# Kernel tuning notes

Hardware: AMD Instinct MI355X
Metric: run time of the kernel (lower is better)

## Reference

```python
import jax, jax.numpy as jnp
import numpy as np

NEG = -1e6  # masked_softmax fill value from the torch source


def setup_inputs() -> dict:
    key = jax.random.key(0)
    ks = jax.random.split(key, 7)
    B, NQ, NK, D, H = 4, 256, 1024, 256, 256
    queries = jax.random.normal(ks[0], (B, NQ, D), dtype=jnp.float32)
    keys_ = jax.random.normal(ks[1], (B, NK, D), dtype=jnp.float32)
    values = jax.random.normal(ks[2], (B, NK, D), dtype=jnp.float32)
    valid_lens = jax.random.randint(ks[3], (B,), 1, NK + 1, dtype=jnp.int32)
    scale = 1.0 / np.sqrt(D)
    Wq = jax.random.normal(ks[4], (D, H), dtype=jnp.float32) * scale
    Wk = jax.random.normal(ks[5], (D, H), dtype=jnp.float32) * scale
    w_v = jax.random.normal(ks[6], (H,), dtype=jnp.float32) * (1.0 / np.sqrt(H))
    return {"queries": queries, "keys": keys_, "values": values,
            "valid_lens": valid_lens, "Wq": Wq, "Wk": Wk, "w_v": w_v}


def reference(queries, keys, values, valid_lens, Wq, Wk, w_v):
    # projections
    q = jnp.einsum('bqd,dh->bqh', queries, Wq)           # [B,NQ,H]
    k = jnp.einsum('bkd,dh->bkh', keys, Wk)              # [B,NK,H]
    # broadcast-add + tanh + dense(->1): scores [B,NQ,NK]
    features = jnp.tanh(q[:, :, None, :] + k[:, None, :, :])  # [B,NQ,NK,H]
    scores = jnp.einsum('bqkh,h->bqk', features, w_v)
    # masked softmax over last axis with per-batch valid lengths
    nk = keys.shape[1]
    mask = jnp.arange(nk)[None, None, :] < valid_lens[:, None, None]  # [B,1,NK]
    scores = jnp.where(mask, scores, NEG)
    attn = jax.nn.softmax(scores, axis=-1)               # [B,NQ,NK]
    # dropout in eval mode -> identity
    return jnp.einsum('bqk,bkd->bqd', attn, values)      # [B,NQ,D]
```

## Files before the change

kernel.cpp:

```cpp
#include <hip/hip_runtime.h>
#include <math.h>

#define BB 4
#define NQ 256
#define NK 1024
#define DD 256
#define HH 256

#define TM 64
#define TN 64
#define TKK 16
#define NT (DD / TKK)

__global__ __launch_bounds__(256) void proj_tanh_kernel(
    const float* __restrict__ Q, const float* __restrict__ K,
    const float* __restrict__ Wq, const float* __restrict__ Wk,
    float* __restrict__ tq, float* __restrict__ tk)
{
    const int QTILES = (BB * NQ) / TM;
    int bx = blockIdx.x;
    const float* A; const float* W; float* C; int bm;
    if (bx < QTILES) { A = Q; W = Wq; C = tq; bm = bx * TM; }
    else             { A = K; W = Wk; C = tk; bm = (bx - QTILES) * TM; }
    int bn = blockIdx.y * TN;

    __shared__ float As[2][TKK][TM + 4];
    __shared__ float Ws[2][TKK][TN + 4];

    int tid = threadIdx.x;
    int ar = tid >> 2, ac4 = tid & 3;
    int wkk = tid >> 4, wc4 = tid & 15;
    int ty = tid >> 4, tx = tid & 15;

    float4 aR = *(const float4*)&A[(size_t)(bm + ar) * DD + ac4 * 4];
    float4 wR = *(const float4*)&W[(size_t)wkk * HH + bn + wc4 * 4];

    float acc[4][4] = {};

    for (int t = 0; t < NT; ++t) {
        int cur = t & 1;
        As[cur][ac4 * 4 + 0][ar] = aR.x;
        As[cur][ac4 * 4 + 1][ar] = aR.y;
        As[cur][ac4 * 4 + 2][ar] = aR.z;
        As[cur][ac4 * 4 + 3][ar] = aR.w;
        *(float4*)&Ws[cur][wkk][wc4 * 4] = wR;
        if (t + 1 < NT) {
            int k0 = (t + 1) * TKK;
            aR = *(const float4*)&A[(size_t)(bm + ar) * DD + k0 + ac4 * 4];
            wR = *(const float4*)&W[(size_t)(k0 + wkk) * HH + bn + wc4 * 4];
        }
        __syncthreads();
#pragma unroll
        for (int kk = 0; kk < TKK; ++kk) {
            float4 a4 = *(const float4*)&As[cur][kk][ty * 4];
            float4 w4 = *(const float4*)&Ws[cur][kk][tx * 4];
            acc[0][0] = fmaf(a4.x, w4.x, acc[0][0]);
            acc[0][1] = fmaf(a4.x, w4.y, acc[0][1]);
            acc[0][2] = fmaf(a4.x, w4.z, acc[0][2]);
            acc[0][3] = fmaf(a4.x, w4.w, acc[0][3]);
            acc[1][0] = fmaf(a4.y, w4.x, acc[1][0]);
            acc[1][1] = fmaf(a4.y, w4.y, acc[1][1]);
            acc[1][2] = fmaf(a4.y, w4.z, acc[1][2]);
            acc[1][3] = fmaf(a4.y, w4.w, acc[1][3]);
            acc[2][0] = fmaf(a4.z, w4.x, acc[2][0]);
            acc[2][1] = fmaf(a4.z, w4.y, acc[2][1]);
            acc[2][2] = fmaf(a4.z, w4.z, acc[2][2]);
            acc[2][3] = fmaf(a4.z, w4.w, acc[2][3]);
            acc[3][0] = fmaf(a4.w, w4.x, acc[3][0]);
            acc[3][1] = fmaf(a4.w, w4.y, acc[3][1]);
            acc[3][2] = fmaf(a4.w, w4.z, acc[3][2]);
            acc[3][3] = fmaf(a4.w, w4.w, acc[3][3]);
        }
    }

#pragma unroll
    for (int i = 0; i < 4; ++i) {
        int m = bm + ty * 4 + i;
        float4 o;
        float t0 = tanhf(acc[i][0]), t1 = tanhf(acc[i][1]);
        float t2 = tanhf(acc[i][2]), t3 = tanhf(acc[i][3]);
        o.x = fminf(fmaxf(t0, -0.999999f), 0.999999f);
        o.y = fminf(fmaxf(t1, -0.999999f), 0.999999f);
        o.z = fminf(fmaxf(t2, -0.999999f), 0.999999f);
        o.w = fminf(fmaxf(t3, -0.999999f), 0.999999f);
        *(float4*)&C[(size_t)m * HH + bn + tx * 4] = o;
    }
}

__device__ __forceinline__ float pairterm(float a1, float b1, float w1,
                                          float a2, float b2, float w2, float acc) {
    float d1 = fmaf(a1, b1, 1.f);
    float d2 = fmaf(a2, b2, 1.f);
    float n1 = w1 * (a1 + b1);
    float n2 = w2 * (a2 + b2);
    float num = fmaf(n2, d1, n1 * d2);
    return fmaf(num, __builtin_amdgcn_rcpf(d1 * d2), acc);
}
__device__ __forceinline__ float pair2(float4 A, float4 B, float4 w, float acc) {
    acc = pairterm(A.x, B.x, w.x, A.y, B.y, w.y, acc);
    acc = pairterm(A.z, B.z, w.z, A.w, B.w, w.w, acc);
    return acc;
}

__global__ __launch_bounds__(256) void scores_kernel(
    const float* __restrict__ tq, const float* __restrict__ tk,
    const float* __restrict__ wv, const int* __restrict__ vlen,
    float* __restrict__ St, float* __restrict__ Psum)
{
    __shared__ __align__(16) float sQ[32][HH + 4];
    __shared__ __align__(16) float sK[32][HH + 4];
    __shared__ __align__(16) float sW[HH];

    int bid = blockIdx.x;
    int b = bid & 3;
    int rest = bid >> 2;
    int qc = rest & 7;
    int kc = rest >> 3;
    int L = vlen[b];
    int k0 = kc * 32;
    if (k0 >= L) return;
    int q0 = qc * 32;

    int tid = threadIdx.x;
    {
        int c4 = tid & 63, r0 = tid >> 6;
        const float4* gq = (const float4*)(tq + ((size_t)b * NQ + q0) * HH);
        const float4* gk = (const float4*)(tk + ((size_t)b * NK + k0) * HH);
#pragma unroll
        for (int r = 0; r < 32; r += 4) {
            *(float4*)&sQ[r + r0][c4 * 4] = gq[(size_t)(r + r0) * (HH / 4) + c4];
            *(float4*)&sK[r + r0][c4 * 4] = gk[(size_t)(r + r0) * (HH / 4) + c4];
        }
        sW[tid] = wv[tid];
    }
    __syncthreads();

    int ki = tid & 15, qi = tid >> 4;
    float a00 = 0.f, a01 = 0.f, a10 = 0.f, a11 = 0.f;
    const float4* qp0 = (const float4*)&sQ[qi][0];
    const float4* qp1 = (const float4*)&sQ[qi + 16][0];
    const float4* kp0 = (const float4*)&sK[ki][0];
    const float4* kp1 = (const float4*)&sK[ki + 16][0];
    const float4* wp  = (const float4*)sW;

#pragma unroll 4
    for (int h = 0; h < HH / 4; ++h) {
        float4 w4 = wp[h];
        float4 A0 = qp0[h], A1 = qp1[h];
        float4 B0 = kp0[h], B1 = kp1[h];
        a00 = pair2(A0, B0, w4, a00);
        a01 = pair2(A0, B1, w4, a01);
        a10 = pair2(A1, B0, w4, a10);
        a11 = pair2(A1, B1, w4, a11);
    }

    int kA = k0 + ki, kB = kA + 16;
    float p00 = (kA < L) ? __expf(a00) : 0.f;
    float p10 = (kA < L) ? __expf(a10) : 0.f;
    float p01 = (kB < L) ? __expf(a01) : 0.f;
    float p11 = (kB < L) ? __expf(a11) : 0.f;

    float* s0 = St + ((size_t)b * NQ + q0 + qi) * NK;
    float* s1 = St + ((size_t)b * NQ + q0 + qi + 16) * NK;
    s0[kA] = p00; s0[kB] = p01;
    s1[kA] = p10; s1[kB] = p11;

    float r0s = p00 + p01, r1s = p10 + p11;
#pragma unroll
    for (int o = 1; o <= 8; o <<= 1) {
        r0s += __shfl_xor(r0s, o, 64);
        r1s += __shfl_xor(r1s, o, 64);
    }
    if (ki == 0) {
        Psum[((size_t)b * NQ + q0 + qi) * 32 + kc] = r0s;
        Psum[((size_t)b * NQ + q0 + qi + 16) * 32 + kc] = r1s;
    }
}

__global__ __launch_bounds__(256) void pv_kernel(
    const float* __restrict__ St, const float* __restrict__ V,
    const float* __restrict__ Psum, const int* __restrict__ vlen,
    float* __restrict__ out)
{
    __shared__ __align__(16) float sPt[2][32][36];
    __shared__ __align__(16) float sV[2][32][36];
    __shared__ float sAll[3][64][17];
    __shared__ float sRowsum[32];

    int bid = blockIdx.x;
    int b = bid & 3;
    int rest = bid >> 2;
    int qt = rest >> 3, dt = rest & 7;
    int q0 = qt * 32, d0 = dt * 32;
    int L = vlen[b];
    int nc = (L + 31) >> 5;

    int tid = threadIdx.x;
    if (tid < 32) {
        float s = 0.f;
        const float* pp = Psum + ((size_t)b * NQ + q0 + tid) * 32;
        for (int c = 0; c < nc; ++c) s += pp[c];
        sRowsum[tid] = s;
    }

    int r = tid >> 3, c4 = tid & 7;
    int w = tid >> 6, sp = tid & 63;
    int qg = sp >> 3, dg = sp & 7;

    const float* Stb = St + ((size_t)b * NQ + q0 + r) * NK;
    const float* Vb  = V + (size_t)b * NK * DD + d0;

    float4 pf = *(const float4*)(Stb + c4 * 4);
    float4 vf = *(const float4*)(Vb + (size_t)r * DD + c4 * 4);

    float acc[4][4] = {};

    for (int c = 0; c < nc; ++c) {
        int cur = c & 1;
        sPt[cur][c4 * 4 + 0][r] = pf.x;
        sPt[cur][c4 * 4 + 1][r] = pf.y;
        sPt[cur][c4 * 4 + 2][r] = pf.z;
        sPt[cur][c4 * 4 + 3][r] = pf.w;
        *(float4*)&sV[cur][r][c4 * 4] = vf;
        if (c + 1 < nc) {
            int kn = (c + 1) * 32;
            pf = *(const float4*)(Stb + kn + c4 * 4);
            vf = *(const float4*)(Vb + (size_t)(kn + r) * DD + c4 * 4);
        }
        __syncthreads();
#pragma unroll
        for (int kk = 0; kk < 8; ++kk) {
            float4 A  = *(const float4*)&sPt[cur][w * 8 + kk][qg * 4];
            float4 Bv = *(const float4*)&sV[cur][w * 8 + kk][dg * 4];
            acc[0][0] = fmaf(A.x, Bv.x, acc[0][0]);
            acc[0][1] = fmaf(A.x, Bv.y, acc[0][1]);
            acc[0][2] = fmaf(A.x, Bv.z, acc[0][2]);
            acc[0][3] = fmaf(A.x, Bv.w, acc[0][3]);
            acc[1][0] = fmaf(A.y, Bv.x, acc[1][0]);
            acc[1][1] = fmaf(A.y, Bv.y, acc[1][1]);
            acc[1][2] = fmaf(A.y, Bv.z, acc[1][2]);
            acc[1][3] = fmaf(A.y, Bv.w, acc[1][3]);
            acc[2][0] = fmaf(A.z, Bv.x, acc[2][0]);
            acc[2][1] = fmaf(A.z, Bv.y, acc[2][1]);
            acc[2][2] = fmaf(A.z, Bv.z, acc[2][2]);
            acc[2][3] = fmaf(A.z, Bv.w, acc[2][3]);
            acc[3][0] = fmaf(A.w, Bv.x, acc[3][0]);
            acc[3][1] = fmaf(A.w, Bv.y, acc[3][1]);
            acc[3][2] = fmaf(A.w, Bv.z, acc[3][2]);
            acc[3][3] = fmaf(A.w, Bv.w, acc[3][3]);
        }
    }

    if (w > 0) {
#pragma unroll
        for (int i = 0; i < 4; ++i)
#pragma unroll
            for (int j = 0; j < 4; ++j) sAll[w - 1][sp][i * 4 + j] = acc[i][j];
    }
    __syncthreads();
    if (w == 0) {
#pragma unroll
        for (int ww = 0; ww < 3; ++ww)
#pragma unroll
            for (int i = 0; i < 4; ++i)
#pragma unroll
                for (int j = 0; j < 4; ++j) acc[i][j] += sAll[ww][sp][i * 4 + j];
#pragma unroll
        for (int i = 0; i < 4; ++i) {
            float inv = 1.0f / sRowsum[qg * 4 + i];
            float4 o = { acc[i][0] * inv, acc[i][1] * inv,
                         acc[i][2] * inv, acc[i][3] * inv };
            *(float4*)&out[((size_t)b * NQ + q0 + qg * 4 + i) * DD + d0 + dg * 4] = o;
        }
    }
}

extern "C" void kernel_launch(void* const* d_in, const int* in_sizes, int n_in,
                              void* d_out, int out_size, void* d_ws, size_t ws_size,
                              hipStream_t stream) {
    const float* queries = (const float*)d_in[0];
    const float* keys    = (const float*)d_in[1];
    const float* values  = (const float*)d_in[2];
    const int*   vlens   = (const int*)d_in[3];
    const float* Wq      = (const float*)d_in[4];
    const float* Wk      = (const float*)d_in[5];
    const float* wv      = (const float*)d_in[6];
    float* out = (float*)d_out;

    float* tq   = (float*)d_ws;
    float* tk   = tq + (size_t)BB * NQ * HH;
    float* St   = tk + (size_t)BB * NK * HH;
    float* Psum = St + (size_t)BB * NQ * NK;

    dim3 pgrid((BB * NQ) / TM + (BB * NK) / TM, HH / TN);
    proj_tanh_kernel<<<pgrid, 256, 0, stream>>>(queries, keys, Wq, Wk, tq, tk);

    scores_kernel<<<dim3(BB * (NQ / 32) * (NK / 32)), 256, 0, stream>>>(
        tq, tk, wv, vlens, St, Psum);

    pv_kernel<<<dim3(BB * (NQ / 32) * (DD / 32)), 256, 0, stream>>>(
        St, values, Psum, vlens, out);
}
```

Measured before the change: 60.64 us.

## Use exp-domain tanh identity, split H across blocks, add combine kernel

The projection epilogue now stores exp(2x), clamped, in place of tanh(x). The score kernel evaluates sum w*tanh(q+k) through the identity tanh(a+b) = 1 - 2/(1+e^{2a}e^{2b}), computed as rational pairs with one reciprocal per four h terms. The H dimension is split into four chunks over more 64x64 blocks, so partial sums go to a new buffer. A new combine kernel reduces those partials and applies exp and the row sums, and key tiles past the valid length are skipped in the projection. The cost is extra global traffic for the four partial score planes, one more launch, and clamping the pre-activation to ±8, which changes accuracy slightly.

```diff
diff --git a/kernel.cpp b/kernel.cpp
--- a/kernel.cpp
+++ b/kernel.cpp
@@ -12,16 +12,23 @@
 #define TKK 16
 #define NT (DD / TKK)
 
-__global__ __launch_bounds__(256) void proj_tanh_kernel(
+__global__ __launch_bounds__(256) void proj_exp_kernel(
     const float* __restrict__ Q, const float* __restrict__ K,
     const float* __restrict__ Wq, const float* __restrict__ Wk,
-    float* __restrict__ tq, float* __restrict__ tk)
+    const int* __restrict__ vlen,
+    float* __restrict__ Eq, float* __restrict__ Ek)
 {
     const int QTILES = (BB * NQ) / TM;
     int bx = blockIdx.x;
     const float* A; const float* W; float* C; int bm;
-    if (bx < QTILES) { A = Q; W = Wq; C = tq; bm = bx * TM; }
-    else             { A = K; W = Wk; C = tk; bm = (bx - QTILES) * TM; }
+    if (bx < QTILES) { A = Q; W = Wq; C = Eq; bm = bx * TM; }
+    else {
+        int kt = bx - QTILES;
+        int b = kt >> 4;
+        int lr = (kt & 15) * TM;
+        if (lr >= vlen[b]) return;
+        A = K; W = Wk; C = Ek; bm = kt * TM;
+    }
     int bn = blockIdx.y * TN;
 
     __shared__ float As[2][TKK][TM + 4];
@@ -71,121 +78,142 @@
             acc[3][2] = fmaf(a4.w, w4.z, acc[3][2]);
             acc[3][3] = fmaf(a4.w, w4.w, acc[3][3]);
         }
+        __syncthreads();
     }
 
 #pragma unroll
     for (int i = 0; i < 4; ++i) {
         int m = bm + ty * 4 + i;
         float4 o;
-        float t0 = tanhf(acc[i][0]), t1 = tanhf(acc[i][1]);
-        float t2 = tanhf(acc[i][2]), t3 = tanhf(acc[i][3]);
-        o.x = fminf(fmaxf(t0, -0.999999f), 0.999999f);
-        o.y = fminf(fmaxf(t1, -0.999999f), 0.999999f);
-        o.z = fminf(fmaxf(t2, -0.999999f), 0.999999f);
-        o.w = fminf(fmaxf(t3, -0.999999f), 0.999999f);
+        o.x = __expf(2.f * fminf(fmaxf(acc[i][0], -8.f), 8.f));
+        o.y = __expf(2.f * fminf(fmaxf(acc[i][1], -8.f), 8.f));
+        o.z = __expf(2.f * fminf(fmaxf(acc[i][2], -8.f), 8.f));
+        o.w = __expf(2.f * fminf(fmaxf(acc[i][3], -8.f), 8.f));
         *(float4*)&C[(size_t)m * HH + bn + tx * 4] = o;
     }
 }
 
-__device__ __forceinline__ float pairterm(float a1, float b1, float w1,
-                                          float a2, float b2, float w2, float acc) {
-    float d1 = fmaf(a1, b1, 1.f);
-    float d2 = fmaf(a2, b2, 1.f);
-    float n1 = w1 * (a1 + b1);
-    float n2 = w2 * (a2 + b2);
-    float num = fmaf(n2, d1, n1 * d2);
-    return fmaf(num, __builtin_amdgcn_rcpf(d1 * d2), acc);
-}
-__device__ __forceinline__ float pair2(float4 A, float4 B, float4 w, float acc) {
-    acc = pairterm(A.x, B.x, w.x, A.y, B.y, w.y, acc);
-    acc = pairterm(A.z, B.z, w.z, A.w, B.w, w.w, acc);
-    return acc;
-}
+#define SH 64
+#define NHC (HH / SH)
 
 __global__ __launch_bounds__(256) void scores_kernel(
-    const float* __restrict__ tq, const float* __restrict__ tk,
+    const float* __restrict__ Eq, const float* __restrict__ Ek,
     const float* __restrict__ wv, const int* __restrict__ vlen,
-    float* __restrict__ St, float* __restrict__ Psum)
+    float* __restrict__ Tpart)
 {
-    __shared__ __align__(16) float sQ[32][HH + 4];
-    __shared__ __align__(16) float sK[32][HH + 4];
-    __shared__ __align__(16) float sW[HH];
+    __shared__ __align__(16) float sQ[64][SH + 4];
+    __shared__ __align__(16) float sK[64][SH + 4];
+    __shared__ float sW[SH];
 
     int bid = blockIdx.x;
-    int b = bid & 3;
-    int rest = bid >> 2;
-    int qc = rest & 7;
-    int kc = rest >> 3;
+    int b  = bid & 3;
+    int qc = (bid >> 2) & 3;
+    int kc = (bid >> 4) & 15;
+    int hc = bid >> 8;
     int L = vlen[b];
-    int k0 = kc * 32;
+    int k0 = kc * 64;
     if (k0 >= L) return;
-    int q0 = qc * 32;
+    int q0 = qc * 64, h0 = hc * SH;
 
     int tid = threadIdx.x;
     {
-        int c4 = tid & 63, r0 = tid >> 6;
-        const float4* gq = (const float4*)(tq + ((size_t)b * NQ + q0) * HH);
-        const float4* gk = (const float4*)(tk + ((size_t)b * NK + k0) * HH);
-#pragma unroll
-        for (int r = 0; r < 32; r += 4) {
-            *(float4*)&sQ[r + r0][c4 * 4] = gq[(size_t)(r + r0) * (HH / 4) + c4];
-            *(float4*)&sK[r + r0][c4 * 4] = gk[(size_t)(r + r0) * (HH / 4) + c4];
-        }
-        sW[tid] = wv[tid];
+        int rr0 = tid >> 4;
+        int c4  = tid & 15;
+        const float* gq = Eq + ((size_t)b * NQ + q0) * HH + h0;
+        const float* gk = Ek + ((size_t)b * NK + k0) * HH + h0;
+#pragma unroll
+        for (int rr = 0; rr < 4; ++rr) {
+            int r = rr0 + rr * 16;
+            *(float4*)&sQ[r][c4 * 4] = *(const float4*)&gq[(size_t)r * HH + c4 * 4];
+            *(float4*)&sK[r][c4 * 4] = *(const float4*)&gk[(size_t)r * HH + c4 * 4];
+        }
+        if (tid < SH) sW[tid] = wv[h0 + tid];
     }
     __syncthreads();
 
-    int ki = tid & 15, qi = tid >> 4;
-    float a00 = 0.f, a01 = 0.f, a10 = 0.f, a11 = 0.f;
-    const float4* qp0 = (const float4*)&sQ[qi][0];
-    const float4* qp1 = (const float4*)&sQ[qi + 16][0];
-    const float4* kp0 = (const float4*)&sK[ki][0];
-    const float4* kp1 = (const float4*)&sK[ki + 16][0];
-    const float4* wp  = (const float4*)sW;
-
-#pragma unroll 4
-    for (int h = 0; h < HH / 4; ++h) {
-        float4 w4 = wp[h];
-        float4 A0 = qp0[h], A1 = qp1[h];
-        float4 B0 = kp0[h], B1 = kp1[h];
-        a00 = pair2(A0, B0, w4, a00);
-        a01 = pair2(A0, B1, w4, a01);
-        a10 = pair2(A1, B0, w4, a10);
-        a11 = pair2(A1, B1, w4, a11);
-    }
-
-    int kA = k0 + ki, kB = kA + 16;
-    float p00 = (kA < L) ? __expf(a00) : 0.f;
-    float p10 = (kA < L) ? __expf(a10) : 0.f;
-    float p01 = (kB < L) ? __expf(a01) : 0.f;
-    float p11 = (kB < L) ? __expf(a11) : 0.f;
-
-    float* s0 = St + ((size_t)b * NQ + q0 + qi) * NK;
-    float* s1 = St + ((size_t)b * NQ + q0 + qi + 16) * NK;
-    s0[kA] = p00; s0[kB] = p01;
-    s1[kA] = p10; s1[kB] = p11;
-
-    float r0s = p00 + p01, r1s = p10 + p11;
-#pragma unroll
-    for (int o = 1; o <= 8; o <<= 1) {
-        r0s += __shfl_xor(r0s, o, 64);
-        r1s += __shfl_xor(r1s, o, 64);
-    }
-    if (ki == 0) {
-        Psum[((size_t)b * NQ + q0 + qi) * 32 + kc] = r0s;
-        Psum[((size_t)b * NQ + q0 + qi + 16) * 32 + kc] = r1s;
-    }
+    int qi = tid >> 4, ki = tid & 15;
+    float acc[4][4] = {};
+
+    for (int h4 = 0; h4 < SH / 4; ++h4) {
+        float4 w = *(const float4*)&sW[h4 * 4];
+        float wxy = w.x + w.y, wzw = w.z + w.w;
+        float4 Aq[4], Bk[4];
+#pragma unroll
+        for (int i = 0; i < 4; ++i) Aq[i] = *(const float4*)&sQ[qi + 16 * i][h4 * 4];
+#pragma unroll
+        for (int j = 0; j < 4; ++j) Bk[j] = *(const float4*)&sK[ki + 16 * j][h4 * 4];
+#pragma unroll
+        for (int i = 0; i < 4; ++i)
+#pragma unroll
+            for (int j = 0; j < 4; ++j) {
+                float4 a = Aq[i], e = Bk[j];
+                float E1 = a.x * e.x, E2 = a.y * e.y;
+                float E3 = a.z * e.z, E4 = a.w * e.w;
+                float d1 = E1 + 1.f, d2 = E2 + 1.f;
+                float d3 = E3 + 1.f, d4 = E4 + 1.f;
+                float n12 = fmaf(w.x, E2, fmaf(w.y, E1, wxy));
+                float n34 = fmaf(w.z, E4, fmaf(w.w, E3, wzw));
+                float d12 = d1 * d2, d34 = d3 * d4;
+                float num = fmaf(n12, d34, n34 * d12);
+                acc[i][j] = fmaf(num, __builtin_amdgcn_rcpf(d12 * d34), acc[i][j]);
+            }
+    }
+
+    float* Tb = Tpart + (size_t)hc * (BB * NQ * NK)
+              + ((size_t)b * NQ + q0) * NK + k0;
+#pragma unroll
+    for (int i = 0; i < 4; ++i)
+#pragma unroll
+        for (int j = 0; j < 4; ++j)
+            Tb[(size_t)(qi + 16 * i) * NK + ki + 16 * j] = acc[i][j];
+}
+
+__global__ __launch_bounds__(256) void combine_kernel(
+    const float* __restrict__ Tpart, const int* __restrict__ vlen,
+    float* __restrict__ P, float* __restrict__ Psum)
+{
+    __shared__ float sRed[4];
+    int row = blockIdx.x;
+    int b = row >> 8;
+    int L = vlen[b];
+    int tid = threadIdx.x;
+    const size_t stride = (size_t)BB * NQ * NK;
+    const float* T0 = Tpart + (size_t)row * NK;
+
+    int k = tid * 4;
+    float4 p = {0.f, 0.f, 0.f, 0.f};
+    if (k < L) {
+        float4 t0 = *(const float4*)&T0[k];
+        float4 t1 = *(const float4*)&T0[stride + k];
+        float4 t2 = *(const float4*)&T0[2 * stride + k];
+        float4 t3 = *(const float4*)&T0[3 * stride + k];
+        float Tx = (t0.x + t1.x) + (t2.x + t3.x);
+        float Ty = (t0.y + t1.y) + (t2.y + t3.y);
+        float Tz = (t0.z + t1.z) + (t2.z + t3.z);
+        float Tw = (t0.w + t1.w) + (t2.w + t3.w);
+        p.x = __expf(-2.f * Tx);
+        p.y = (k + 1 < L) ? __expf(-2.f * Ty) : 0.f;
+        p.z = (k + 2 < L) ? __expf(-2.f * Tz) : 0.f;
+        p.w = (k + 3 < L) ? __expf(-2.f * Tw) : 0.f;
+    }
+    *(float4*)&P[(size_t)row * NK + k] = p;
+
+    float s = (p.x + p.y) + (p.z + p.w);
+#pragma unroll
+    for (int o = 32; o; o >>= 1) s += __shfl_xor(s, o, 64);
+    if ((tid & 63) == 0) sRed[tid >> 6] = s;
+    __syncthreads();
+    if (tid == 0) Psum[row] = (sRed[0] + sRed[1]) + (sRed[2] + sRed[3]);
 }
 
 __global__ __launch_bounds__(256) void pv_kernel(
-    const float* __restrict__ St, const float* __restrict__ V,
+    const float* __restrict__ P, const float* __restrict__ V,
     const float* __restrict__ Psum, const int* __restrict__ vlen,
     float* __restrict__ out)
 {
     __shared__ __align__(16) float sPt[2][32][36];
     __shared__ __align__(16) float sV[2][32][36];
     __shared__ float sAll[3][64][17];
-    __shared__ float sRowsum[32];
 
     int bid = blockIdx.x;
     int b = bid & 3;
@@ -196,21 +224,14 @@
     int nc = (L + 31) >> 5;
 
     int tid = threadIdx.x;
-    if (tid < 32) {
-        float s = 0.f;
-        const float* pp = Psum + ((size_t)b * NQ + q0 + tid) * 32;
-        for (int c = 0; c < nc; ++c) s += pp[c];
-        sRowsum[tid] = s;
-    }
-
     int r = tid >> 3, c4 = tid & 7;
     int w = tid >> 6, sp = tid & 63;
     int qg = sp >> 3, dg = sp & 7;
 
-    const float* Stb = St + ((size_t)b * NQ + q0 + r) * NK;
-    const float* Vb  = V + (size_t)b * NK * DD + d0;
-
-    float4 pf = *(const float4*)(Stb + c4 * 4);
+    const float* Pb = P + ((size_t)b * NQ + q0 + r) * NK;
+    const float* Vb = V + (size_t)b * NK * DD + d0;
+
+    float4 pf = *(const float4*)(Pb + c4 * 4);
     float4 vf = *(const float4*)(Vb + (size_t)r * DD + c4 * 4);
 
     float acc[4][4] = {};
@@ -224,7 +245,7 @@
         *(float4*)&sV[cur][r][c4 * 4] = vf;
         if (c + 1 < nc) {
             int kn = (c + 1) * 32;
-            pf = *(const float4*)(Stb + kn + c4 * 4);
+            pf = *(const float4*)(Pb + kn + c4 * 4);
             vf = *(const float4*)(Vb + (size_t)(kn + r) * DD + c4 * 4);
         }
         __syncthreads();
@@ -249,6 +270,7 @@
             acc[3][2] = fmaf(A.w, Bv.z, acc[3][2]);
             acc[3][3] = fmaf(A.w, Bv.w, acc[3][3]);
         }
+        __syncthreads();
     }
 
     if (w > 0) {
@@ -267,7 +289,7 @@
                 for (int j = 0; j < 4; ++j) acc[i][j] += sAll[ww][sp][i * 4 + j];
 #pragma unroll
         for (int i = 0; i < 4; ++i) {
-            float inv = 1.0f / sRowsum[qg * 4 + i];
+            float inv = 1.0f / Psum[(size_t)b * NQ + q0 + qg * 4 + i];
             float4 o = { acc[i][0] * inv, acc[i][1] * inv,
                          acc[i][2] * inv, acc[i][3] * inv };
             *(float4*)&out[((size_t)b * NQ + q0 + qg * 4 + i) * DD + d0 + dg * 4] = o;
@@ -287,17 +309,21 @@
     const float* wv      = (const float*)d_in[6];
     float* out = (float*)d_out;
 
-    float* tq   = (float*)d_ws;
-    float* tk   = tq + (size_t)BB * NQ * HH;
-    float* St   = tk + (size_t)BB * NK * HH;
-    float* Psum = St + (size_t)BB * NQ * NK;
+    float* Eqb   = (float*)d_ws;
+    float* Ekb   = Eqb + (size_t)BB * NQ * HH;
+    float* Tpart = Ekb + (size_t)BB * NK * HH;
+    float* P     = Tpart + (size_t)NHC * BB * NQ * NK;
+    float* Psum  = P + (size_t)BB * NQ * NK;
 
     dim3 pgrid((BB * NQ) / TM + (BB * NK) / TM, HH / TN);
-    proj_tanh_kernel<<<pgrid, 256, 0, stream>>>(queries, keys, Wq, Wk, tq, tk);
-
-    scores_kernel<<<dim3(BB * (NQ / 32) * (NK / 32)), 256, 0, stream>>>(
-        tq, tk, wv, vlens, St, Psum);
+    proj_exp_kernel<<<pgrid, 256, 0, stream>>>(queries, keys, Wq, Wk, vlens,
+                                               Eqb, Ekb);
+
+    scores_kernel<<<dim3(4 * 4 * 16 * NHC), 256, 0, stream>>>(
+        Eqb, Ekb, wv, vlens, Tpart);
+
+    combine_kernel<<<dim3(BB * NQ), 256, 0, stream>>>(Tpart, vlens, P, Psum);
 
     pv_kernel<<<dim3(BB * (NQ / 32) * (DD / 32)), 256, 0, stream>>>(
-        St, values, Psum, vlens, out);
-}
+        P, values, Psum, vlens, out);
+}
```

Measured after the change: 62.43 us. 1.03x slower.

## Reformulate tanh-sum via exponentials, skip masked key projection tiles, add loop barriers

Applied to the files above, without the earlier changes.

The projection now stores exp(2x) of the clamped projections instead of tanh. The scores loop then uses the identity tanh(a+b) = 1 - 2/(1+e^{2a}e^{2b}), folding four h-terms into one reciprocal, and the softmax exponent is adjusted to match. Projection tiles for keys beyond the batch's valid length are skipped early. Trailing __syncthreads are added in the double-buffered loops to fix a shared-memory race, at the cost of extra barriers. The ±8 clamp and the product of four (1+E) factors could lose precision or overflow.

```diff
diff --git a/kernel.cpp b/kernel.cpp
--- a/kernel.cpp
+++ b/kernel.cpp
@@ -12,16 +12,23 @@
 #define TKK 16
 #define NT (DD / TKK)
 
-__global__ __launch_bounds__(256) void proj_tanh_kernel(
+__global__ __launch_bounds__(256) void proj_exp_kernel(
     const float* __restrict__ Q, const float* __restrict__ K,
     const float* __restrict__ Wq, const float* __restrict__ Wk,
-    float* __restrict__ tq, float* __restrict__ tk)
+    const int* __restrict__ vlen,
+    float* __restrict__ Eq, float* __restrict__ Ek)
 {
     const int QTILES = (BB * NQ) / TM;
     int bx = blockIdx.x;
     const float* A; const float* W; float* C; int bm;
-    if (bx < QTILES) { A = Q; W = Wq; C = tq; bm = bx * TM; }
-    else             { A = K; W = Wk; C = tk; bm = (bx - QTILES) * TM; }
+    if (bx < QTILES) { A = Q; W = Wq; C = Eq; bm = bx * TM; }
+    else {
+        int kt = bx - QTILES;
+        int b = kt >> 4;
+        int lr = (kt & 15) * TM;
+        if (lr >= vlen[b]) return;
+        A = K; W = Wk; C = Ek; bm = kt * TM;
+    }
     int bn = blockIdx.y * TN;
 
     __shared__ float As[2][TKK][TM + 4];
@@ -71,41 +78,25 @@
             acc[3][2] = fmaf(a4.w, w4.z, acc[3][2]);
             acc[3][3] = fmaf(a4.w, w4.w, acc[3][3]);
         }
+        __syncthreads();
     }
 
 #pragma unroll
     for (int i = 0; i < 4; ++i) {
         int m = bm + ty * 4 + i;
         float4 o;
-        float t0 = tanhf(acc[i][0]), t1 = tanhf(acc[i][1]);
-        float t2 = tanhf(acc[i][2]), t3 = tanhf(acc[i][3]);
-        o.x = fminf(fmaxf(t0, -0.999999f), 0.999999f);
-        o.y = fminf(fmaxf(t1, -0.999999f), 0.999999f);
-        o.z = fminf(fmaxf(t2, -0.999999f), 0.999999f);
-        o.w = fminf(fmaxf(t3, -0.999999f), 0.999999f);
+        o.x = __expf(2.f * fminf(fmaxf(acc[i][0], -8.f), 8.f));
+        o.y = __expf(2.f * fminf(fmaxf(acc[i][1], -8.f), 8.f));
+        o.z = __expf(2.f * fminf(fmaxf(acc[i][2], -8.f), 8.f));
+        o.w = __expf(2.f * fminf(fmaxf(acc[i][3], -8.f), 8.f));
         *(float4*)&C[(size_t)m * HH + bn + tx * 4] = o;
     }
 }
 
-__device__ __forceinline__ float pairterm(float a1, float b1, float w1,
-                                          float a2, float b2, float w2, float acc) {
-    float d1 = fmaf(a1, b1, 1.f);
-    float d2 = fmaf(a2, b2, 1.f);
-    float n1 = w1 * (a1 + b1);
-    float n2 = w2 * (a2 + b2);
-    float num = fmaf(n2, d1, n1 * d2);
-    return fmaf(num, __builtin_amdgcn_rcpf(d1 * d2), acc);
-}
-__device__ __forceinline__ float pair2(float4 A, float4 B, float4 w, float acc) {
-    acc = pairterm(A.x, B.x, w.x, A.y, B.y, w.y, acc);
-    acc = pairterm(A.z, B.z, w.z, A.w, B.w, w.w, acc);
-    return acc;
-}
-
 __global__ __launch_bounds__(256) void scores_kernel(
-    const float* __restrict__ tq, const float* __restrict__ tk,
+    const float* __restrict__ Eq, const float* __restrict__ Ek,
     const float* __restrict__ wv, const int* __restrict__ vlen,
-    float* __restrict__ St, float* __restrict__ Psum)
+    float* __restrict__ P, float* __restrict__ Psum)
 {
     __shared__ __align__(16) float sQ[32][HH + 4];
     __shared__ __align__(16) float sK[32][HH + 4];
@@ -124,8 +115,8 @@
     int tid = threadIdx.x;
     {
         int c4 = tid & 63, r0 = tid >> 6;
-        const float4* gq = (const float4*)(tq + ((size_t)b * NQ + q0) * HH);
-        const float4* gk = (const float4*)(tk + ((size_t)b * NK + k0) * HH);
+        const float4* gq = (const float4*)(Eq + ((size_t)b * NQ + q0) * HH);
+        const float4* gk = (const float4*)(Ek + ((size_t)b * NK + k0) * HH);
 #pragma unroll
         for (int r = 0; r < 32; r += 4) {
             *(float4*)&sQ[r + r0][c4 * 4] = gq[(size_t)(r + r0) * (HH / 4) + c4];
@@ -144,24 +135,38 @@
     const float4* wp  = (const float4*)sW;
 
 #pragma unroll 4
-    for (int h = 0; h < HH / 4; ++h) {
-        float4 w4 = wp[h];
-        float4 A0 = qp0[h], A1 = qp1[h];
-        float4 B0 = kp0[h], B1 = kp1[h];
-        a00 = pair2(A0, B0, w4, a00);
-        a01 = pair2(A0, B1, w4, a01);
-        a10 = pair2(A1, B0, w4, a10);
-        a11 = pair2(A1, B1, w4, a11);
+    for (int h4 = 0; h4 < HH / 4; ++h4) {
+        float4 w = wp[h4];
+        float wxy = w.x + w.y, wzw = w.z + w.w;
+        float4 A0 = qp0[h4], A1 = qp1[h4];
+        float4 B0 = kp0[h4], B1 = kp1[h4];
+#define QUAD(acc, Aq, Bk)                                                    \
+        {                                                                    \
+            float E1 = Aq.x * Bk.x, E2 = Aq.y * Bk.y;                        \
+            float E3 = Aq.z * Bk.z, E4 = Aq.w * Bk.w;                        \
+            float d1 = E1 + 1.f, d2 = E2 + 1.f;                              \
+            float d3 = E3 + 1.f, d4 = E4 + 1.f;                              \
+            float n12 = fmaf(w.x, E2, fmaf(w.y, E1, wxy));                   \
+            float n34 = fmaf(w.z, E4, fmaf(w.w, E3, wzw));                   \
+            float d12 = d1 * d2, d34 = d3 * d4;                              \
+            float num = fmaf(n12, d34, n34 * d12);                           \
+            acc = fmaf(num, __builtin_amdgcn_rcpf(d12 * d34), acc);          \
+        }
+        QUAD(a00, A0, B0);
+        QUAD(a01, A0, B1);
+        QUAD(a10, A1, B0);
+        QUAD(a11, A1, B1);
+#undef QUAD
     }
 
     int kA = k0 + ki, kB = kA + 16;
-    float p00 = (kA < L) ? __expf(a00) : 0.f;
-    float p10 = (kA < L) ? __expf(a10) : 0.f;
-    float p01 = (kB < L) ? __expf(a01) : 0.f;
-    float p11 = (kB < L) ? __expf(a11) : 0.f;
-
-    float* s0 = St + ((size_t)b * NQ + q0 + qi) * NK;
-    float* s1 = St + ((size_t)b * NQ + q0 + qi + 16) * NK;
+    float p00 = (kA < L) ? __expf(-2.f * a00) : 0.f;
+    float p10 = (kA < L) ? __expf(-2.f * a10) : 0.f;
+    float p01 = (kB < L) ? __expf(-2.f * a01) : 0.f;
+    float p11 = (kB < L) ? __expf(-2.f * a11) : 0.f;
+
+    float* s0 = P + ((size_t)b * NQ + q0 + qi) * NK;
+    float* s1 = P + ((size_t)b * NQ + q0 + qi + 16) * NK;
     s0[kA] = p00; s0[kB] = p01;
     s1[kA] = p10; s1[kB] = p11;
 
@@ -178,7 +183,7 @@
 }
 
 __global__ __launch_bounds__(256) void pv_kernel(
-    const float* __restrict__ St, const float* __restrict__ V,
+    const float* __restrict__ P, const float* __restrict__ V,
     const float* __restrict__ Psum, const int* __restrict__ vlen,
     float* __restrict__ out)
 {
@@ -207,10 +212,10 @@
     int w = tid >> 6, sp = tid & 63;
     int qg = sp >> 3, dg = sp & 7;
 
-    const float* Stb = St + ((size_t)b * NQ + q0 + r) * NK;
-    const float* Vb  = V + (size_t)b * NK * DD + d0;
-
-    float4 pf = *(const float4*)(Stb + c4 * 4);
+    const float* Pb = P + ((size_t)b * NQ + q0 + r) * NK;
+    const float* Vb = V + (size_t)b * NK * DD + d0;
+
+    float4 pf = *(const float4*)(Pb + c4 * 4);
     float4 vf = *(const float4*)(Vb + (size_t)r * DD + c4 * 4);
 
     float acc[4][4] = {};
@@ -224,7 +229,7 @@
         *(float4*)&sV[cur][r][c4 * 4] = vf;
         if (c + 1 < nc) {
             int kn = (c + 1) * 32;
-            pf = *(const float4*)(Stb + kn + c4 * 4);
+            pf = *(const float4*)(Pb + kn + c4 * 4);
             vf = *(const float4*)(Vb + (size_t)(kn + r) * DD + c4 * 4);
         }
         __syncthreads();
@@ -249,6 +254,7 @@
             acc[3][2] = fmaf(A.w, Bv.z, acc[3][2]);
             acc[3][3] = fmaf(A.w, Bv.w, acc[3][3]);
         }
+        __syncthreads();
     }
 
     if (w > 0) {
@@ -287,17 +293,18 @@
     const float* wv      = (const float*)d_in[6];
     float* out = (float*)d_out;
 
-    float* tq   = (float*)d_ws;
-    float* tk   = tq + (size_t)BB * NQ * HH;
-    float* St   = tk + (size_t)BB * NK * HH;
-    float* Psum = St + (size_t)BB * NQ * NK;
+    float* Eqb  = (float*)d_ws;
+    float* Ekb  = Eqb + (size_t)BB * NQ * HH;
+    float* P    = Ekb + (size_t)BB * NK * HH;
+    float* Psum = P + (size_t)BB * NQ * NK;
 
     dim3 pgrid((BB * NQ) / TM + (BB * NK) / TM, HH / TN);
-    proj_tanh_kernel<<<pgrid, 256, 0, stream>>>(queries, keys, Wq, Wk, tq, tk);
+    proj_exp_kernel<<<pgrid, 256, 0, stream>>>(queries, keys, Wq, Wk, vlens,
+                                               Eqb, Ekb);
 
     scores_kernel<<<dim3(BB * (NQ / 32) * (NK / 32)), 256, 0, stream>>>(
-        tq, tk, wv, vlens, St, Psum);
+        Eqb, Ekb, wv, vlens, P, Psum);
 
     pv_kernel<<<dim3(BB * (NQ / 32) * (DD / 32)), 256, 0, stream>>>(
-        St, values, Psum, vlens, out);
+        P, values, Psum, vlens, out);
 }
```

Result: faster. 56.14 us (-7.4%).
